# Optimization experiments

Hardware: AMD Instinct MI355X
Metric: run time of the kernel (lower is better)

Reference implementation:

```python
import jax, jax.numpy as jnp
import numpy as np

EPS = 1e-5


def layer_norm(x, g, b):
    m = jnp.mean(x, axis=-1, keepdims=True)
    v = jnp.mean((x - m) ** 2, axis=-1, keepdims=True)
    return (x - m) / jnp.sqrt(v + EPS) * g + b


def rel_shift(x, klen):
    # x: [q, p, b, n] -> Transformer-XL relative shift -> [q, klen, b, n]
    q, p, b, n = x.shape
    x = jnp.reshape(x, (p, q, b, n))
    x = x[1:]
    x = jnp.reshape(x, (q, p - 1, b, n))
    return x[:, :klen]


def setup_inputs() -> dict:
    S, B, D, NH, DH, DF = 1024, 4, 1024, 16, 64, 4096
    key = jax.random.key(0)
    ks = jax.random.split(key, 16)
    w = 0.02  # scale random params for numerical sanity
    return {
        "src": jax.random.normal(ks[0], (S, B, D), jnp.float32),
        "pos_emb": jax.random.normal(ks[1], (S + 1, B, D), jnp.float32),
        "src_mask": jnp.zeros((S, S), dtype=bool),
        "qw": jax.random.normal(ks[2], (D, NH, DH), jnp.float32) * w,
        "kw": jax.random.normal(ks[3], (D, NH, DH), jnp.float32) * w,
        "vw": jax.random.normal(ks[4], (D, NH, DH), jnp.float32) * w,
        "rw": jax.random.normal(ks[5], (D, NH, DH), jnp.float32) * w,
        "ow": jax.random.normal(ks[6], (D, NH, DH), jnp.float32) * w,
        "r_w_bias": jax.random.normal(ks[7], (NH, DH), jnp.float32) * w,
        "r_r_bias": jax.random.normal(ks[8], (NH, DH), jnp.float32) * w,
        "w1": jax.random.normal(ks[9], (DF, D), jnp.float32) * w,
        "b1": jnp.zeros((DF,), jnp.float32),
        "w2": jax.random.normal(ks[10], (D, DF), jnp.float32) * w,
        "b2": jnp.zeros((D,), jnp.float32),
        "g1": jnp.ones((D,), jnp.float32),
        "beta1": jnp.zeros((D,), jnp.float32),
        "g2": jnp.ones((D,), jnp.float32),
        "beta2": jnp.zeros((D,), jnp.float32),
    }


def reference(src, pos_emb, src_mask, qw, kw, vw, rw, ow, r_w_bias, r_r_bias,
              w1, b1, w2, b2, g1, beta1, g2, beta2):
    S = src.shape[0]
    d_head = qw.shape[-1]
    scale = 1.0 / d_head ** 0.5

    # mem=None -> cat == src; dropout layers are identity (eval)
    q_head = jnp.einsum('ibh,hnd->ibnd', src, qw)
    k_head = jnp.einsum('ibh,hnd->ibnd', src, kw)
    v_head = jnp.einsum('ibh,hnd->ibnd', src, vw)
    k_pos = jnp.einsum('ibh,hnd->ibnd', pos_emb, rw)

    ac = jnp.einsum('ibnd,jbnd->ijbn', q_head + r_w_bias, k_head)       # [S,S,B,N]
    bd = jnp.einsum('ibnd,jbnd->ijbn', q_head + r_r_bias, k_pos)        # [S,S+1,B,N]
    bd = rel_shift(bd, klen=S)

    mask = src_mask.astype(ac.dtype)[:, :, None, None]
    attn_score = (ac + bd) * scale - 1e30 * mask
    attn_prob = jax.nn.softmax(attn_score, axis=1)

    attn_vec = jnp.einsum('ijbn,jbnd->ibnd', attn_prob, v_head)
    attn_out = jnp.einsum('ibnd,hnd->ibh', attn_vec, ow)

    x = layer_norm(src + attn_out, g1, beta1)
    ff = jax.nn.gelu(x @ w1.T + b1, approximate=False) @ w2.T + b2
    return layer_norm(x + ff, g2, beta2)
```

## Files before the change

kernel.cpp:

```cpp
#include <hip/hip_runtime.h>
#include <math.h>

typedef __bf16 bf16x8 __attribute__((ext_vector_type(8)));
typedef __bf16 bf16x4 __attribute__((ext_vector_type(4)));
typedef float f32x4 __attribute__((ext_vector_type(4)));

__device__ __forceinline__ void gload_lds16(const __bf16* g, __bf16* l) {
  __builtin_amdgcn_global_load_lds((const __attribute__((address_space(1))) void*)g,
                                   (__attribute__((address_space(3))) void*)l, 16, 0, 0);
}

__device__ __forceinline__ float gelu_exact(float v) {
  return 0.5f * v * (1.f + erff(v * 0.70710678118654752f));
}

__global__ __launch_bounds__(256) void prep_all(
    const float* __restrict__ src, __bf16* __restrict__ srcB2,
    const float* __restrict__ pos, __bf16* __restrict__ posB,
    const float* __restrict__ ow, __bf16* __restrict__ owB,
    const float* __restrict__ w1, __bf16* __restrict__ w1B,
    const float* __restrict__ w2, __bf16* __restrict__ w2B,
    const float* __restrict__ qw, const float* __restrict__ kw,
    const float* __restrict__ vw, const float* __restrict__ rw,
    __bf16* __restrict__ qkvT, __bf16* __restrict__ rwT) {
  __shared__ float t[32][33];
  int bid = blockIdx.x;
  const int tid = threadIdx.x;
  if (bid < 4096) {
    const int i = bid & 1023, b = bid >> 10;
    const float4 v = *(const float4*)(src + ((size_t)(i * 4 + b)) * 1024 + tid * 4);
    bf16x4 o = {(__bf16)v.x, (__bf16)v.y, (__bf16)v.z, (__bf16)v.w};
    *(bf16x4*)(srcB2 + (size_t)bid * 1024 + tid * 4) = o;
    return;
  }
  bid -= 4096;
  if (bid < 3329) {
    const float* in; __bf16* out;
    if (bid < 1025) { in = pos; out = posB; }
    else if (bid < 1281) { bid -= 1025; in = ow; out = owB; }
    else if (bid < 2305) { bid -= 1281; in = w1; out = w1B; }
    else { bid -= 2305; in = w2; out = w2B; }
    const int base = bid * 4096 + tid * 4;
#pragma unroll
    for (int k2 = 0; k2 < 4; ++k2) {
      const int off = base + k2 * 1024;
      float4 v = *(const float4*)(in + off);
      bf16x4 o = {(__bf16)v.x, (__bf16)v.y, (__bf16)v.z, (__bf16)v.w};
      *(bf16x4*)(out + off) = o;
    }
    return;
  }
  bid -= 3329;
  const int z = bid >> 10, rem = bid & 1023;
  const float* in; __bf16* out;
  switch (z) {
    case 0: in = qw; out = qkvT; break;
    case 1: in = kw; out = qkvT + 1024 * 1024; break;
    case 2: in = vw; out = qkvT + 2048 * 1024; break;
    default: in = rw; out = rwT; break;
  }
  const int c0 = (rem & 31) * 32, r0 = (rem >> 5) * 32;
  const int tx = tid & 31, ty = tid >> 5;
  for (int yy = ty; yy < 32; yy += 8)
    t[yy][tx] = in[(size_t)(r0 + yy) * 1024 + c0 + tx];
  __syncthreads();
  for (int yy = ty; yy < 32; yy += 8)
    out[(size_t)(c0 + yy) * 1024 + r0 + tx] = (__bf16)t[tx][yy];
}

template<int BM, int BN, int MODE>
__device__ __forceinline__ void gemm_body(
    const __bf16* __restrict__ A, const __bf16* __restrict__ BT,
    float* __restrict__ Cf, __bf16* __restrict__ Cb,
    const float* __restrict__ bias, int M, int N, int K,
    int kStart, int kChunk, int mBase, int nBase, char* smemRaw) {
  constexpr int BK = 32;
  constexpr int ALOAD = (BM * BK) / 2048;
  constexpr int BLOAD = (BN * BK) / 2048;
  __bf16* lA = (__bf16*)smemRaw;
  __bf16* lB = (__bf16*)(smemRaw + 4 * BM * BK);
  const int tid = threadIdx.x;
  const int w = tid >> 6, l = tid & 63;
  const int lr = l & 15, lk = l >> 4;
  const int srow = tid >> 2;
  const int scol = (tid & 3) * 8;
  const int wbase = w * 512;

  const __bf16* aSrc[ALOAD];
  const __bf16* bSrc[BLOAD];
#pragma unroll
  for (int i = 0; i < ALOAD; ++i) {
    int grow = mBase + srow + i * 64;
    grow = grow < M ? grow : M - 1;
    aSrc[i] = A + (size_t)grow * K + kStart + scol;
  }
#pragma unroll
  for (int i = 0; i < BLOAD; ++i) {
    const int grow = nBase + srow + i * 64;
    bSrc[i] = BT + (size_t)grow * K + kStart + scol;
  }
  auto stage = [&](int buf) {
#pragma unroll
    for (int i = 0; i < ALOAD; ++i) {
      gload_lds16(aSrc[i], &lA[buf * BM * BK + i * 2048 + wbase]);
      aSrc[i] += BK;
    }
#pragma unroll
    for (int i = 0; i < BLOAD; ++i) {
      gload_lds16(bSrc[i], &lB[buf * BN * BK + i * 2048 + wbase]);
      bSrc[i] += BK;
    }
  };

  constexpr int WM = BM / 2, WN = BN / 2;
  constexpr int MF = WM / 16, NF = WN / 16;
  const int wr = w >> 1, wc = w & 1;
  f32x4 acc[MF][NF] = {};

  const int nIter = kChunk / BK;
  stage(0);
  int cur = 0;
#pragma unroll 1
  for (int t = 0; t < nIter; ++t) {
    __syncthreads();
    if (t + 1 < nIter) stage(cur ^ 1);
    bf16x8 af[MF], bfr[NF];
#pragma unroll
    for (int mi = 0; mi < MF; ++mi)
      af[mi] = *(const bf16x8*)&lA[cur * BM * BK + (wr * WM + mi * 16 + lr) * BK + lk * 8];
#pragma unroll
    for (int nj = 0; nj < NF; ++nj)
      bfr[nj] = *(const bf16x8*)&lB[cur * BN * BK + (wc * WN + nj * 16 + lr) * BK + lk * 8];
#pragma unroll
    for (int mi = 0; mi < MF; ++mi)
#pragma unroll
      for (int nj = 0; nj < NF; ++nj)
        acc[mi][nj] = __builtin_amdgcn_mfma_f32_16x16x32_bf16(af[mi], bfr[nj], acc[mi][nj], 0, 0, 0);
    cur ^= 1;
  }
#pragma unroll
  for (int mi = 0; mi < MF; ++mi) {
#pragma unroll
    for (int nj = 0; nj < NF; ++nj) {
      const int col = nBase + wc * WN + nj * 16 + lr;
      const int row0 = mBase + wr * WM + mi * 16 + lk * 4;
#pragma unroll
      for (int j = 0; j < 4; ++j) {
        const int row = row0 + j;
        if (row < M) {
          float v = acc[mi][nj][j];
          if constexpr (MODE == 1) {
            v = gelu_exact(v + bias[col]);
            Cb[(size_t)row * N + col] = (__bf16)v;
          } else if constexpr (MODE == 2) {
            Cb[(size_t)row * N + col] = (__bf16)v;
          } else {
            Cf[(size_t)row * N + col] = v;
          }
        }
      }
    }
  }
}

template<int BM, int BN, int MODE>
__global__ __launch_bounds__(256)
void gemm_bt(const __bf16* __restrict__ A, const __bf16* __restrict__ BT,
             float* __restrict__ Cf, __bf16* __restrict__ Cb,
             __bf16* __restrict__ Cb2, const float* __restrict__ bias,
             int M, int N, int K, int kChunk) {
  __shared__ __align__(16) char smem[4 * (BM + BN) * 32];
  __bf16* cb = (blockIdx.z == 1) ? Cb2 : Cb;
  const int gx = gridDim.x;
  const int G = gx * gridDim.y;
  const int flat = blockIdx.y * gx + blockIdx.x;
  const int band = G >> 3;
  const int x8 = flat & 7, loc = flat >> 3;
  const int rpb = band / gx;
  const int ny = x8 * rpb + loc % rpb;
  const int nx = loc / rpb;
  gemm_body<BM, BN, MODE>(A, BT, Cf, cb, bias, M, N, K, blockIdx.z * kChunk,
                          kChunk, ny * BM, nx * BN, smem);
}

__global__ __launch_bounds__(256)
void proj2_kernel(const __bf16* __restrict__ vwT, const __bf16* __restrict__ srcB2,
                  const __bf16* __restrict__ posB, const __bf16* __restrict__ rwT,
                  __bf16* __restrict__ vTB, __bf16* __restrict__ kposB) {
  __shared__ __align__(16) char smem[4 * (128 + 64) * 32];
  const int raw = blockIdx.x;
  int bid = (raw & 7) * 130 + (raw >> 3);
  if (bid < 512) {
    gemm_body<128, 64, 2>(vwT, srcB2, nullptr, vTB, nullptr, 1024, 4096, 1024,
                          0, 1024, (bid >> 6) * 128, (bid & 63) * 64, smem);
  } else {
    const int t = bid - 512;
    gemm_body<128, 64, 2>(posB, rwT, nullptr, kposB, nullptr, 4100, 1024, 1024,
                          0, 1024, (t >> 4) * 128, (t & 15) * 64, smem);
  }
}

template<int MODE>
__global__ __launch_bounds__(512)
void gemm256(const __bf16* __restrict__ A, const __bf16* __restrict__ BT,
             __bf16* __restrict__ Cb, const float* __restrict__ bias,
             int M, int N, int K) {
  __shared__ __align__(16) __bf16 sm[3 * 24576];
  const int tid = threadIdx.x;
  const int wid = tid >> 6, l = tid & 63;
  const int lcol = l & 15, lk = l >> 4;
  const int wm = wid >> 1, wn = wid & 1;
  const int gx = gridDim.x;
  const int G = gx * gridDim.y;
  const int flat = blockIdx.y * gx + blockIdx.x;
  const int band = G >> 3;
  const int x8 = flat & 7, loc = flat >> 3;
  const int rpb = band / gx;
  const int ny = x8 * rpb + loc % rpb;
  const int nx = loc / rpb;
  const int mBase = ny * 256, nBase = nx * 128;

  int rowj[2], gslotj[2];
#pragma unroll
  for (int j = 0; j < 2; ++j) {
    const int u = (wid * 2 + j) * 64 + l;
    rowj[j] = u >> 3;
    gslotj[j] = (u & 7) ^ (rowj[j] & 7);
  }
  auto issueHT = [&](int kt, int ht, int side) {
    __bf16* base = sm + side * 24576 + (ht == 2 ? 16384 : ht * 8192);
#pragma unroll
    for (int j = 0; j < 2; ++j) {
      const __bf16* src = (ht < 2)
        ? A + (size_t)(mBase + ht * 128 + rowj[j]) * K + kt * 64 + gslotj[j] * 8
        : BT + (size_t)(nBase + rowj[j]) * K + kt * 64 + gslotj[j] * 8;
      gload_lds16(src, base + (wid * 2 + j) * 512);
    }
  };

  const int nkt = K >> 6;
  issueHT(0, 0, 0); issueHT(0, 1, 0); issueHT(0, 2, 0);
  issueHT(1, 0, 1); issueHT(1, 1, 1); issueHT(1, 2, 1);

  f32x4 acc[4][4] = {};
#pragma unroll 1
  for (int j = 0; j < nkt; ++j) {
    asm volatile("s_waitcnt vmcnt(6)" ::: "memory");
    __builtin_amdgcn_s_barrier();
    __builtin_amdgcn_sched_barrier(0);
    const int side = j % 3;
    const int sn = (j + 2) % 3;
    const int ktn = (j + 2 < nkt) ? j + 2 : nkt - 1;
    const __bf16* Ab = sm + side * 24576;
    const __bf16* Bb = Ab + 16384;
    issueHT(ktn, 0, sn);
    bf16x8 af[4][2];
#pragma unroll
    for (int mi = 0; mi < 4; ++mi)
#pragma unroll
      for (int kk = 0; kk < 2; ++kk) {
        const int row = wm * 64 + mi * 16 + lcol;
        af[mi][kk] = *(const bf16x8*)&Ab[row * 64 + (((kk * 4 + lk) ^ (row & 7)) * 8)];
      }
    issueHT(ktn, 1, sn);
    bf16x8 bfv[4][2];
#pragma unroll
    for (int nj = 0; nj < 4; ++nj)
#pragma unroll
      for (int kk = 0; kk < 2; ++kk) {
        const int row = wn * 64 + nj * 16 + lcol;
        bfv[nj][kk] = *(const bf16x8*)&Bb[row * 64 + (((kk * 4 + lk) ^ (row & 7)) * 8)];
      }
    issueHT(ktn, 2, sn);
    __builtin_amdgcn_s_setprio(1);
#pragma unroll
    for (int mi = 0; mi < 4; ++mi)
#pragma unroll
      for (int nj = 0; nj < 4; ++nj) {
        acc[mi][nj] = __builtin_amdgcn_mfma_f32_16x16x32_bf16(af[mi][0], bfv[nj][0], acc[mi][nj], 0, 0, 0);
        acc[mi][nj] = __builtin_amdgcn_mfma_f32_16x16x32_bf16(af[mi][1], bfv[nj][1], acc[mi][nj], 0, 0, 0);
      }
    __builtin_amdgcn_s_setprio(0);
  }
#pragma unroll
  for (int mi = 0; mi < 4; ++mi)
#pragma unroll
    for (int nj = 0; nj < 4; ++nj) {
      const int col = nBase + wn * 64 + nj * 16 + lcol;
      const int row0 = mBase + wm * 64 + mi * 16 + lk * 4;
#pragma unroll
      for (int jj = 0; jj < 4; ++jj) {
        float v = acc[mi][nj][jj];
        if constexpr (MODE == 1) v = gelu_exact(v + bias[col]);
        Cb[(size_t)(row0 + jj) * N + col] = (__bf16)v;
      }
    }
}

template<int MODE>
__global__ __launch_bounds__(512)
void gemm512(const __bf16* __restrict__ A, const __bf16* __restrict__ BT,
             __bf16* __restrict__ Cb, const float* __restrict__ bias,
             int M, int N, int K) {
  __shared__ __align__(16) __bf16 sm[2 * 32768];
  const int tid = threadIdx.x;
  const int w = tid >> 6, l = tid & 63;
  const int lcol = l & 15, lk = l >> 4;
  const int wm = w >> 2, wn = w & 3;
  const int gx = gridDim.x;
  const int G = gx * gridDim.y;
  const int flat = blockIdx.y * gx + blockIdx.x;
  const int band = G >> 3;
  const int x8 = flat & 7, loc = flat >> 3;
  const int rpb = band / gx;
  const int ny = x8 * rpb + loc % rpb;
  const int nx = loc / rpb;
  const int mBase = ny * 256, nBase = nx * 256;

  const int rT = tid >> 3;
  const int gslot = ((tid & 7) ^ (rT & 7)) * 8;
  auto stage = [&](int side, int kt) {
#pragma unroll
    for (int i = 0; i < 4; ++i) {
      gload_lds16(A + (size_t)(mBase + i * 64 + rT) * K + kt * 64 + gslot,
                  sm + side * 32768 + i * 4096 + w * 512);
      gload_lds16(BT + (size_t)(nBase + i * 64 + rT) * K + kt * 64 + gslot,
                  sm + side * 32768 + 16384 + i * 4096 + w * 512);
    }
  };

  f32x4 acc[8][4] = {};
  const int nIter = K >> 6;
  stage(0, 0);
  int cur = 0;
#pragma unroll 1
  for (int t = 0; t < nIter; ++t) {
    __syncthreads();
    if (t + 1 < nIter) stage(cur ^ 1, t + 1);
    const __bf16* Ab = sm + cur * 32768;
    const __bf16* Bb = Ab + 16384;
    bf16x8 bfv[4][2];
#pragma unroll
    for (int nj = 0; nj < 4; ++nj)
#pragma unroll
      for (int kk = 0; kk < 2; ++kk) {
        const int row = wn * 64 + nj * 16 + lcol;
        bfv[nj][kk] = *(const bf16x8*)&Bb[row * 64 + (((kk * 4 + lk) ^ (row & 7)) * 8)];
      }
    __builtin_amdgcn_s_setprio(1);
#pragma unroll
    for (int mi = 0; mi < 8; ++mi) {
      const int row = wm * 128 + mi * 16 + lcol;
      bf16x8 a0 = *(const bf16x8*)&Ab[row * 64 + ((lk ^ (row & 7)) * 8)];
      bf16x8 a1 = *(const bf16x8*)&Ab[row * 64 + (((4 + lk) ^ (row & 7)) * 8)];
#pragma unroll
      for (int nj = 0; nj < 4; ++nj) {
        acc[mi][nj] = __builtin_amdgcn_mfma_f32_16x16x32_bf16(a0, bfv[nj][0], acc[mi][nj], 0, 0, 0);
        acc[mi][nj] = __builtin_amdgcn_mfma_f32_16x16x32_bf16(a1, bfv[nj][1], acc[mi][nj], 0, 0, 0);
      }
    }
    __builtin_amdgcn_s_setprio(0);
    cur ^= 1;
  }
#pragma unroll
  for (int mi = 0; mi < 8; ++mi)
#pragma unroll
    for (int nj = 0; nj < 4; ++nj) {
      const int col = nBase + wn * 64 + nj * 16 + lcol;
      const int row0 = mBase + wm * 128 + mi * 16 + lk * 4;
#pragma unroll
      for (int jj = 0; jj < 4; ++jj) {
        float v = acc[mi][nj][jj];
        if constexpr (MODE == 1) v = gelu_exact(v + bias[col]);
        Cb[(size_t)(row0 + jj) * N + col] = (__bf16)v;
      }
    }
}

__global__ __launch_bounds__(256)
void attn8(const __bf16* __restrict__ qk, const __bf16* __restrict__ vT,
           const __bf16* __restrict__ kpos, const float* __restrict__ rwbias,
           const float* __restrict__ rrbias, __bf16* __restrict__ av) {
  constexpr float ALPHA = 0.125f * 1.44269504088896f;
  constexpr int PB = 132;
  __shared__ __align__(16) char smem[74240];
  __bf16* sP  = (__bf16*)(smem + 49152);
  __bf16* sbd = (__bf16*)(smem + 57344);

  const int flat = blockIdx.x;
  const int xcd = flat & 7, rr_ = flat >> 3;
  const int bn = xcd * 8 + (rr_ >> 4);
  const int it = rr_ & 15;
  const int b = bn >> 4, n = bn & 15;
  const int i0 = it * 64;
  const int tid = threadIdx.x;
  const int l = tid & 63;
  const int lcol = l & 15, lk = l >> 4;
  const int strip = (tid >> 6) * 16;
  const int wbase = tid & 192;
  const int nh64 = n * 64;
  const int q = strip + lcol;

  const int rB = tid >> 3;
  const int cs8 = ((tid & 7) ^ (rB & 7)) * 8;

  bf16x8 onesf;
#pragma unroll
  for (int u = 0; u < 8; ++u) onesf[u] = (__bf16)1.0f;

  bf16x8 qac[2], qlo[2], qhi[2];
  {
    const __bf16* qrow = qk + ((size_t)(b * 1024 + i0 + q)) * 2048 + nh64;
    int gH = i0 + q + 1; gH = gH < 1024 ? gH : 1023;
    const __bf16* qrowH = qk + ((size_t)(b * 1024 + gH)) * 2048 + nh64;
#pragma unroll
    for (int kk = 0; kk < 2; ++kk) {
      bf16x8 qv = *(const bf16x8*)(qrow + kk * 32 + lk * 8);
      bf16x8 qh = *(const bf16x8*)(qrowH + kk * 32 + lk * 8);
      const int dbase = nh64 + kk * 32 + lk * 8;
#pragma unroll
      for (int u = 0; u < 8; ++u) {
        const float rb = rrbias[dbase + u];
        qac[kk][u] = (__bf16)(((float)qv[u] + rwbias[dbase + u]) * ALPHA);
        qlo[kk][u] = (__bf16)(((float)qv[u] + rb) * ALPHA);
        qhi[kk][u] = (__bf16)(((float)qh[u] + rb) * ALPHA);
      }
    }
  }

#pragma unroll
  for (int kq = 0; kq < 2; ++kq) {
    const int r = kq * 32 + rB;
    const int dst = (kq * 256 + wbase) * 8;
    gload_lds16(kpos + ((size_t)((960 - i0 + r) * 4 + b)) * 1024 + nh64 + cs8,
                (__bf16*)(smem + 40960) + dst);
    gload_lds16(qk + ((size_t)(b * 1024 + r)) * 2048 + 1024 + nh64 + cs8,
                (__bf16*)(smem) + dst);
    const int rrel = r - i0;
    const int idx = (rrel <= 0) ? (1024 + rrel) : (rrel - 1);
    gload_lds16(kpos + ((size_t)(idx * 4 + b)) * 1024 + nh64 + cs8,
                (__bf16*)(smem + 16384) + dst);
    gload_lds16(vT + ((size_t)(nh64 + r)) * 4096 + b * 1024 + cs8,
                (__bf16*)(smem + 32768) + dst);
  }
  __syncthreads();
  {
    __bf16* kpl = (__bf16*)(smem + 40960);
    const int colb0 = (-i0 - 64) & 127;
#pragma unroll
    for (int fb = 0; fb < 4; ++fb) {
      const int row = fb * 16 + lcol;
      f32x4 g = {};
#pragma unroll
      for (int kk = 0; kk < 2; ++kk) {
        bf16x8 a = *(const bf16x8*)&kpl[row * 64 + (((kk * 4 + lk) ^ (lcol & 7)) * 8)];
        g = __builtin_amdgcn_mfma_f32_16x16x32_bf16(a, qlo[kk], g, 0, 0, 0);
      }
      bf16x4 gw = {(__bf16)g[0], (__bf16)g[1], (__bf16)g[2], (__bf16)g[3]};
      *(bf16x4*)&sbd[q * PB + ((colb0 + fb * 16 + lk * 4) & 127)] = gw;
    }
  }
  __syncthreads();

  f32x4 oacc[4] = {};
  f32x4 zq = {};
  size_t kS = (size_t)(b * 1024 + 64 + rB) * 2048 + 1024 + nh64 + cs8;
  size_t vS = (size_t)(nh64 + rB) * 4096 + b * 1024 + 64 + cs8;

#pragma unroll 1
  for (int jt = 0; jt < 16; ++jt) {
    const int cur = jt & 1, nxt = cur ^ 1;
    const int d0 = jt * 64 - i0;
    __bf16* sK   = (__bf16*)(smem + cur * 8192);
    __bf16* sKn  = (__bf16*)(smem + nxt * 8192);
    __bf16* sKP  = (__bf16*)(smem + 16384 + cur * 8192);
    __bf16* sKPn = (__bf16*)(smem + 16384 + nxt * 8192);
    __bf16* sVT  = (__bf16*)(smem + 32768 + cur * 8192);
    __bf16* sVTn = (__bf16*)(smem + 32768 + nxt * 8192);
#pragma unroll
    for (int kq = 0; kq < 2; ++kq) {
      const int dst = (kq * 256 + wbase) * 8;
      gload_lds16(qk + kS + kq * 65536, sKn + dst);
      gload_lds16(vT + vS + kq * 131072, sVTn + dst);
      const int rreln = d0 + 64 + kq * 32 + rB;
      const int idx = (rreln <= 0) ? (1024 + rreln) : (rreln - 1);
      gload_lds16(kpos + ((size_t)(idx * 4 + b)) * 1024 + nh64 + cs8, sKPn + dst);
    }
    kS += 131072; vS += 64;
    {
      const bf16x8 qg0 = (d0 >= 0) ? qhi[0] : qlo[0];
      const bf16x8 qg1 = (d0 >= 0) ? qhi[1] : qlo[1];
#pragma unroll
      for (int fb = 0; fb < 4; ++fb) {
        const int row = fb * 16 + lcol;
        f32x4 g = {};
        g = __builtin_amdgcn_mfma_f32_16x16x32_bf16(
            *(const bf16x8*)&sKP[row * 64 + ((lk ^ (lcol & 7)) * 8)], qg0, g, 0, 0, 0);
        g = __builtin_amdgcn_mfma_f32_16x16x32_bf16(
            *(const bf16x8*)&sKP[row * 64 + (((4 + lk) ^ (lcol & 7)) * 8)], qg1, g, 0, 0, 0);
        bf16x4 gw = {(__bf16)g[0], (__bf16)g[1], (__bf16)g[2], (__bf16)g[3]};
        *(bf16x4*)&sbd[q * PB + ((d0 + fb * 16 + lk * 4) & 127)] = gw;
      }
      if (d0 == 0) {
        const int cl = tid >> 2, part = tid & 3;
        const __bf16* qs = qk + ((size_t)(b * 1024 + i0 + cl)) * 2048 + nh64 + part * 16;
        bf16x8 a0 = *(const bf16x8*)qs;
        bf16x8 a1 = *(const bf16x8*)(qs + 8);
        bf16x8 k0 = *(const bf16x8*)&sKP[(2 * part) * 8];
        bf16x8 k1 = *(const bf16x8*)&sKP[(2 * part + 1) * 8];
        float s64 = 0.f;
#pragma unroll
        for (int u = 0; u < 8; ++u)
          s64 += ((float)a0[u] + rrbias[nh64 + part * 16 + u]) * (float)k0[u]
               + ((float)a1[u] + rrbias[nh64 + part * 16 + 8 + u]) * (float)k1[u];
        s64 += __shfl_xor(s64, 1, 64);
        s64 += __shfl_xor(s64, 2, 64);
        if (part == 0) sbd[cl * PB] = (__bf16)(s64 * ALPHA);
      }
    }
    f32x4 sc[4];
#pragma unroll
    for (int fk = 0; fk < 4; ++fk) {
      const int row = fk * 16 + lcol;
      f32x4 a = {};
#pragma unroll
      for (int kk = 0; kk < 2; ++kk) {
        bf16x8 kf = *(const bf16x8*)&sK[row * 64 + (((kk * 4 + lk) ^ (lcol & 7)) * 8)];
        a = __builtin_amdgcn_mfma_f32_16x16x32_bf16(kf, qac[kk], a, 0, 0, 0);
      }
      sc[fk] = a;
    }
    {
      const int rowb = q * PB;
      const int sb = d0 - q;
#pragma unroll
      for (int fk = 0; fk < 4; ++fk) {
        const int cb = sb + fk * 16 + lk * 4;
        float e0 = exp2f(sc[fk][0] + (float)sbd[rowb + ((cb) & 127)]);
        float e1 = exp2f(sc[fk][1] + (float)sbd[rowb + ((cb + 1) & 127)]);
        float e2 = exp2f(sc[fk][2] + (float)sbd[rowb + ((cb + 2) & 127)]);
        float e3 = exp2f(sc[fk][3] + (float)sbd[rowb + ((cb + 3) & 127)]);
        bf16x4 pw = {(__bf16)e0, (__bf16)e1, (__bf16)e2, (__bf16)e3};
        *(bf16x4*)&sP[q * 64 + (((fk * 2 + (lk >> 1)) ^ (q & 7)) * 8) + (lk & 1) * 4] = pw;
      }
    }
#pragma unroll
    for (int kk = 0; kk < 2; ++kk) {
      bf16x8 pa = *(const bf16x8*)&sP[q * 64 + (((kk * 4 + lk) ^ (q & 7)) * 8)];
      zq = __builtin_amdgcn_mfma_f32_16x16x32_bf16(pa, onesf, zq, 0, 0, 0);
#pragma unroll
      for (int fd = 0; fd < 4; ++fd) {
        const int vrow = fd * 16 + lcol;
        bf16x8 bv = *(const bf16x8*)&sVT[vrow * 64 + (((kk * 4 + lk) ^ (lcol & 7)) * 8)];
        oacc[fd] = __builtin_amdgcn_mfma_f32_16x16x32_bf16(pa, bv, oacc[fd], 0, 0, 0);
      }
    }
    __syncthreads();
  }
#pragma unroll
  for (int jj = 0; jj < 4; ++jj) {
    const float rz = 1.f / zq[jj];
    const int ig = i0 + strip + lk * 4 + jj;
    __bf16* dst = av + ((size_t)(ig * 4 + b)) * 1024 + nh64;
#pragma unroll
    for (int fd = 0; fd < 4; ++fd)
      dst[fd * 16 + lcol] = (__bf16)(oacc[fd][jj] * rz);
  }
}

__global__ __launch_bounds__(256)
void ln_fuse(const float* __restrict__ A, const __bf16* __restrict__ P0,
             const __bf16* __restrict__ P1, const float* __restrict__ cb,
             const float* __restrict__ g, const float* __restrict__ be,
             float* __restrict__ oF, __bf16* __restrict__ oB) {
  const int row = blockIdx.x, t = threadIdx.x;
  const size_t base = (size_t)row * 1024 + t * 4;
  const float4 a = *(const float4*)(A + base);
  const bf16x4 p0 = *(const bf16x4*)(P0 + base);
  const bf16x4 p1 = *(const bf16x4*)(P1 + base);
  float x0 = a.x + (float)p0[0] + (float)p1[0];
  float x1 = a.y + (float)p0[1] + (float)p1[1];
  float x2 = a.z + (float)p0[2] + (float)p1[2];
  float x3 = a.w + (float)p0[3] + (float)p1[3];
  if (cb) {
    const float4 c = *(const float4*)(cb + t * 4);
    x0 += c.x; x1 += c.y; x2 += c.z; x3 += c.w;
  }
  float s = x0 + x1 + x2 + x3;
  float qq = x0 * x0 + x1 * x1 + x2 * x2 + x3 * x3;
#pragma unroll
  for (int o = 1; o < 64; o <<= 1) { s += __shfl_xor(s, o, 64); qq += __shfl_xor(qq, o, 64); }
  __shared__ float ss[4], qs[4];
  if ((t & 63) == 0) { ss[t >> 6] = s; qs[t >> 6] = qq; }
  __syncthreads();
  s = ss[0] + ss[1] + ss[2] + ss[3];
  qq = qs[0] + qs[1] + qs[2] + qs[3];
  const float mean = s * (1.f / 1024.f);
  const float var = qq * (1.f / 1024.f) - mean * mean;
  const float rstd = rsqrtf(var + 1e-5f);
  const float4 gv = *(const float4*)(g + t * 4);
  const float4 bev = *(const float4*)(be + t * 4);
  const float y0 = (x0 - mean) * rstd * gv.x + bev.x;
  const float y1 = (x1 - mean) * rstd * gv.y + bev.y;
  const float y2 = (x2 - mean) * rstd * gv.z + bev.z;
  const float y3 = (x3 - mean) * rstd * gv.w + bev.w;
  if (oF) {
    float4 r = {y0, y1, y2, y3};
    *(float4*)(oF + base) = r;
  }
  if (oB) {
    bf16x4 o4 = {(__bf16)y0, (__bf16)y1, (__bf16)y2, (__bf16)y3};
    *(bf16x4*)(oB + base) = o4;
  }
}

extern "C" void kernel_launch(void* const* d_in, const int* in_sizes, int n_in,
                              void* d_out, int out_size, void* d_ws, size_t ws_size,
                              hipStream_t stream) {
  const float* src    = (const float*)d_in[0];
  const float* pos    = (const float*)d_in[1];
  const float* qw     = (const float*)d_in[3];
  const float* kw     = (const float*)d_in[4];
  const float* vw     = (const float*)d_in[5];
  const float* rw     = (const float*)d_in[6];
  const float* ow     = (const float*)d_in[7];
  const float* rwbias = (const float*)d_in[8];
  const float* rrbias = (const float*)d_in[9];
  const float* w1     = (const float*)d_in[10];
  const float* b1     = (const float*)d_in[11];
  const float* w2     = (const float*)d_in[12];
  const float* b2     = (const float*)d_in[13];
  const float* g1     = (const float*)d_in[14];
  const float* be1    = (const float*)d_in[15];
  const float* g2     = (const float*)d_in[16];
  const float* be2    = (const float*)d_in[17];
  float* out = (float*)d_out;

  char* p = (char*)d_ws;
  auto alloc = [&](size_t bytes) { char* r = p; p += (bytes + 255) & ~(size_t)255; return r; };
  __bf16* qkB   = (__bf16*)alloc(4096ull * 2048 * 2);
  __bf16* vTB   = (__bf16*)alloc(1024ull * 4096 * 2);
  __bf16* kposB = (__bf16*)alloc(4100ull * 1024 * 2);
  __bf16* avB   = (__bf16*)alloc(4096ull * 1024 * 2);
  __bf16* srcB2 = (__bf16*)alloc(4096ull * 1024 * 2);
  __bf16* posB  = (__bf16*)alloc(4100ull * 1024 * 2);
  float*  xF    = (float*)alloc(4096ull * 1024 * 4);
  __bf16* w2B   = (__bf16*)alloc(4096ull * 1024 * 2);
  __bf16* qkvT  = (__bf16*)alloc(3072ull * 1024 * 2);
  __bf16* rwT   = (__bf16*)alloc(1024ull * 1024 * 2);
  __bf16* owB   = (__bf16*)alloc(1024ull * 1024 * 2);
  __bf16* w1B   = (__bf16*)alloc(4096ull * 1024 * 2);
  __bf16* xB    = (__bf16*)alloc(4096ull * 1024 * 2);
  __bf16* gB   = qkB;
  __bf16* aoP0 = srcB2;
  __bf16* aoP1 = posB;
  __bf16* ffP0 = avB;
  __bf16* ffP1 = w1B;

  prep_all<<<11521, 256, 0, stream>>>(src, srcB2, pos, posB, ow, owB, w1, w1B,
                                      w2, w2B, qw, kw, vw, rw, qkvT, rwT);
  gemm256<2><<<dim3(16, 16), 512, 0, stream>>>(srcB2, qkvT, qkB, nullptr, 4096, 2048, 1024);
  proj2_kernel<<<1040, 256, 0, stream>>>(qkvT + 2048 * 1024, srcB2, posB, rwT, vTB, kposB);
  attn8<<<dim3(1024), 256, 0, stream>>>(qkB, vTB, kposB, rwbias, rrbias, avB);
  gemm_bt<128, 64, 2><<<dim3(16, 32, 2), 256, 0, stream>>>(avB, owB, nullptr, aoP0, aoP1, nullptr, 4096, 1024, 1024, 512);
  ln_fuse<<<4096, 256, 0, stream>>>(src, aoP0, aoP1, nullptr, g1, be1, xF, xB);
  gemm512<1><<<dim3(16, 16), 512, 0, stream>>>(xB, w1B, gB, b1, 4096, 4096, 1024);
  gemm_bt<128, 64, 2><<<dim3(16, 32, 2), 256, 0, stream>>>(gB, w2B, nullptr, ffP0, ffP1, nullptr, 4096, 1024, 4096, 2048);
  ln_fuse<<<4096, 256, 0, stream>>>(xF, ffP0, ffP1, b2, g2, be2, out, nullptr);
  (void)in_sizes; (void)n_in; (void)out_size; (void)ws_size;
}
```

Measured before the change: 307.6 us.

## Run FFN down-projection on 256x256 GEMM with 4-way split-K; raise MFMA priority in attention

The second FFN GEMM moves from the 128x64 two-way split-K kernel to the 256x256 512-thread GEMM. That kernel gains a K-chunk offset and four output pointers, so it runs as a 4-way split-K. The final layer-norm kernel now sums four bf16 partial buffers instead of two. This is meant to raise data reuse per tile while keeping enough blocks in flight. The cost is extra partial-sum traffic, and one partial is written into the reused qkvT buffer, which is smaller than 4096x1024 and so relies on spilling into the adjacent rwT allocation. Separately, s_setprio is raised around the MFMA blocks in the attention loop to favour matrix-instruction issue.

```diff
diff --git a/kernel.cpp b/kernel.cpp
--- a/kernel.cpp
+++ b/kernel.cpp
@@ -300,8 +300,9 @@
 template<int MODE>
 __global__ __launch_bounds__(512)
 void gemm512(const __bf16* __restrict__ A, const __bf16* __restrict__ BT,
-             __bf16* __restrict__ Cb, const float* __restrict__ bias,
-             int M, int N, int K) {
+             __bf16* __restrict__ Cb0, __bf16* __restrict__ Cb1,
+             __bf16* __restrict__ Cb2, __bf16* __restrict__ Cb3,
+             const float* __restrict__ bias, int M, int N, int K, int kChunk) {
   __shared__ __align__(16) __bf16 sm[2 * 32768];
   const int tid = threadIdx.x;
   const int w = tid >> 6, l = tid & 63;
@@ -316,21 +317,24 @@
   const int ny = x8 * rpb + loc % rpb;
   const int nx = loc / rpb;
   const int mBase = ny * 256, nBase = nx * 256;
+  const int kStart = blockIdx.z * kChunk;
+  __bf16* Cb = (blockIdx.z == 0) ? Cb0 : (blockIdx.z == 1) ? Cb1
+             : (blockIdx.z == 2) ? Cb2 : Cb3;
 
   const int rT = tid >> 3;
   const int gslot = ((tid & 7) ^ (rT & 7)) * 8;
   auto stage = [&](int side, int kt) {
 #pragma unroll
     for (int i = 0; i < 4; ++i) {
-      gload_lds16(A + (size_t)(mBase + i * 64 + rT) * K + kt * 64 + gslot,
+      gload_lds16(A + (size_t)(mBase + i * 64 + rT) * K + kStart + kt * 64 + gslot,
                   sm + side * 32768 + i * 4096 + w * 512);
-      gload_lds16(BT + (size_t)(nBase + i * 64 + rT) * K + kt * 64 + gslot,
+      gload_lds16(BT + (size_t)(nBase + i * 64 + rT) * K + kStart + kt * 64 + gslot,
                   sm + side * 32768 + 16384 + i * 4096 + w * 512);
     }
   };
 
   f32x4 acc[8][4] = {};
-  const int nIter = K >> 6;
+  const int nIter = kChunk >> 6;
   stage(0, 0);
   int cur = 0;
 #pragma unroll 1
@@ -490,6 +494,7 @@
     {
       const bf16x8 qg0 = (d0 >= 0) ? qhi[0] : qlo[0];
       const bf16x8 qg1 = (d0 >= 0) ? qhi[1] : qlo[1];
+      __builtin_amdgcn_s_setprio(1);
 #pragma unroll
       for (int fb = 0; fb < 4; ++fb) {
         const int row = fb * 16 + lcol;
@@ -501,6 +506,7 @@
         bf16x4 gw = {(__bf16)g[0], (__bf16)g[1], (__bf16)g[2], (__bf16)g[3]};
         *(bf16x4*)&sbd[q * PB + ((d0 + fb * 16 + lk * 4) & 127)] = gw;
       }
+      __builtin_amdgcn_s_setprio(0);
       if (d0 == 0) {
         const int cl = tid >> 2, part = tid & 3;
         const __bf16* qs = qk + ((size_t)(b * 1024 + i0 + cl)) * 2048 + nh64 + part * 16;
@@ -519,6 +525,7 @@
       }
     }
     f32x4 sc[4];
+    __builtin_amdgcn_s_setprio(1);
 #pragma unroll
     for (int fk = 0; fk < 4; ++fk) {
       const int row = fk * 16 + lcol;
@@ -530,6 +537,7 @@
       }
       sc[fk] = a;
     }
+    __builtin_amdgcn_s_setprio(0);
     {
       const int rowb = q * PB;
       const int sb = d0 - q;
@@ -544,6 +552,7 @@
         *(bf16x4*)&sP[q * 64 + (((fk * 2 + (lk >> 1)) ^ (q & 7)) * 8) + (lk & 1) * 4] = pw;
       }
     }
+    __builtin_amdgcn_s_setprio(1);
 #pragma unroll
     for (int kk = 0; kk < 2; ++kk) {
       bf16x8 pa = *(const bf16x8*)&sP[q * 64 + (((kk * 4 + lk) ^ (q & 7)) * 8)];
@@ -555,6 +564,7 @@
         oacc[fd] = __builtin_amdgcn_mfma_f32_16x16x32_bf16(pa, bv, oacc[fd], 0, 0, 0);
       }
     }
+    __builtin_amdgcn_s_setprio(0);
     __syncthreads();
   }
 #pragma unroll
@@ -570,7 +580,8 @@
 
 __global__ __launch_bounds__(256)
 void ln_fuse(const float* __restrict__ A, const __bf16* __restrict__ P0,
-             const __bf16* __restrict__ P1, const float* __restrict__ cb,
+             const __bf16* __restrict__ P1, const __bf16* __restrict__ P2,
+             const __bf16* __restrict__ P3, const float* __restrict__ cb,
              const float* __restrict__ g, const float* __restrict__ be,
              float* __restrict__ oF, __bf16* __restrict__ oB) {
   const int row = blockIdx.x, t = threadIdx.x;
@@ -582,6 +593,14 @@
   float x1 = a.y + (float)p0[1] + (float)p1[1];
   float x2 = a.z + (float)p0[2] + (float)p1[2];
   float x3 = a.w + (float)p0[3] + (float)p1[3];
+  if (P2) {
+    const bf16x4 p2 = *(const bf16x4*)(P2 + base);
+    const bf16x4 p3 = *(const bf16x4*)(P3 + base);
+    x0 += (float)p2[0] + (float)p3[0];
+    x1 += (float)p2[1] + (float)p3[1];
+    x2 += (float)p2[2] + (float)p3[2];
+    x3 += (float)p2[3] + (float)p3[3];
+  }
   if (cb) {
     const float4 c = *(const float4*)(cb + t * 4);
     x0 += c.x; x1 += c.y; x2 += c.z; x3 += c.w;
@@ -656,6 +675,10 @@
   __bf16* aoP1 = posB;
   __bf16* ffP0 = avB;
   __bf16* ffP1 = w1B;
+  __bf16* ffP2 = kposB;
+  __bf16* ffP3 = xB;
+
+  ffP2 = qkvT;
 
   prep_all<<<11521, 256, 0, stream>>>(src, srcB2, pos, posB, ow, owB, w1, w1B,
                                       w2, w2B, qw, kw, vw, rw, qkvT, rwT);
@@ -663,9 +686,9 @@
   proj2_kernel<<<1040, 256, 0, stream>>>(qkvT + 2048 * 1024, srcB2, posB, rwT, vTB, kposB);
   attn8<<<dim3(1024), 256, 0, stream>>>(qkB, vTB, kposB, rwbias, rrbias, avB);
   gemm_bt<128, 64, 2><<<dim3(16, 32, 2), 256, 0, stream>>>(avB, owB, nullptr, aoP0, aoP1, nullptr, 4096, 1024, 1024, 512);
-  ln_fuse<<<4096, 256, 0, stream>>>(src, aoP0, aoP1, nullptr, g1, be1, xF, xB);
-  gemm512<1><<<dim3(16, 16), 512, 0, stream>>>(xB, w1B, gB, b1, 4096, 4096, 1024);
-  gemm_bt<128, 64, 2><<<dim3(16, 32, 2), 256, 0, stream>>>(gB, w2B, nullptr, ffP0, ffP1, nullptr, 4096, 1024, 4096, 2048);
-  ln_fuse<<<4096, 256, 0, stream>>>(xF, ffP0, ffP1, b2, g2, be2, out, nullptr);
+  ln_fuse<<<4096, 256, 0, stream>>>(src, aoP0, aoP1, nullptr, nullptr, nullptr, g1, be1, xF, xB);
+  gemm512<1><<<dim3(16, 16), 512, 0, stream>>>(xB, w1B, gB, nullptr, nullptr, nullptr, b1, 4096, 4096, 1024, 1024);
+  gemm512<2><<<dim3(4, 16, 4), 512, 0, stream>>>(gB, w2B, ffP0, ffP1, ffP2, ffP3, nullptr, 4096, 1024, 4096, 1024);
+  ln_fuse<<<4096, 256, 0, stream>>>(xF, ffP0, ffP1, ffP2, ffP3, b2, g2, be2, out, nullptr);
   (void)in_sizes; (void)n_in; (void)out_size; (void)ws_size;
 }
```

After: 290.7 us. 5.5% less time.
